# Kernel tuning notes

Measured on AMD Instinct MI355X. Metric: run time of the kernel, lower is better.

Reference implementation:

```python
import jax, jax.numpy as jnp
import numpy as np

N_NODES = 50000
N_EDGES = 200000
N_GRAPH = 1024
H = 128          # hidden_channels
POS = 48         # pos_offset
NF = 256         # num_filters in SchNetInteraction
L = 5            # n_layers
NFF = 512
MAX_ITEM = 300


def ssp(v):
    # shifted softplus used by SchNet
    return jax.nn.softplus(v) - jnp.log(2.0)


def setup_inputs() -> dict:
    key = jax.random.key(0)
    ks = iter(jax.random.split(key, 40))
    s = 0.05
    inp = {}
    inp['x'] = jax.random.randint(next(ks), (N_NODES,), 0, MAX_ITEM)
    inp['edge_index'] = jax.random.randint(next(ks), (2, N_EDGES), 0, N_NODES)
    inp['edge_attr'] = jax.random.normal(next(ks), (N_EDGES, 4), jnp.float32)
    inp['batch'] = jnp.sort(jax.random.randint(next(ks), (N_NODES,), 0, N_GRAPH))
    inp['pos'] = jax.random.normal(next(ks), (N_NODES, 3), jnp.float32)
    # embedding / projection params
    vert = jax.random.normal(next(ks), (MAX_ITEM + 1, H - POS), jnp.float32) * s
    inp['vert_emb'] = vert.at[MAX_ITEM].set(0.0)  # padding_idx
    inp['pos_w'] = jax.random.normal(next(ks), (POS, 3), jnp.float32) * s
    inp['edge_w'] = jax.random.normal(next(ks), (H, 4), jnp.float32) * s
    # per-layer SchNetInteraction params (stacked over L)
    inp['filt_w1'] = jax.random.normal(next(ks), (L, NF, H), jnp.float32) * s
    inp['filt_b1'] = jnp.zeros((L, NF), jnp.float32)
    inp['filt_w2'] = jax.random.normal(next(ks), (L, NF, NF), jnp.float32) * s
    inp['filt_b2'] = jnp.zeros((L, NF), jnp.float32)
    inp['lin1_w'] = jax.random.normal(next(ks), (L, NF, H), jnp.float32) * s
    inp['lin2_w'] = jax.random.normal(next(ks), (L, H, NF), jnp.float32) * s
    inp['lin2_b'] = jnp.zeros((L, H), jnp.float32)
    inp['lin3_w'] = jax.random.normal(next(ks), (L, H, H), jnp.float32) * s
    inp['lin3_b'] = jnp.zeros((L, H), jnp.float32)
    # per-layer edge MLP: Linear(edge_ch + in_ch -> in_ch) + Tanh
    inp['em_w'] = jax.random.normal(next(ks), (L, H, 2 * H), jnp.float32) * s
    inp['em_b'] = jnp.zeros((L, H), jnp.float32)
    # head
    inp['head_w1'] = jax.random.normal(next(ks), (NFF, H), jnp.float32) * s
    inp['head_b1'] = jnp.zeros((NFF,), jnp.float32)
    inp['head_w2'] = jax.random.normal(next(ks), (1, NFF), jnp.float32) * s
    inp['head_b2'] = jnp.zeros((1,), jnp.float32)
    return inp


def _forward(x, edge_index, edge_attr, batch, pos, vert_emb, pos_w, edge_w,
             filt_w1, filt_b1, filt_w2, filt_b2, lin1_w, lin2_w, lin2_b,
             lin3_w, lin3_b, em_w, em_b, head_w1, head_b1, head_w2, head_b2):
    n = x.shape[0]
    src, dst = edge_index[0], edge_index[1]
    h = jnp.concatenate([vert_emb[x], pos @ pos_w.T], axis=-1)  # [N, H]
    ea = edge_attr @ edge_w.T                                    # [E, H]
    for i in range(L):
        # SchNetInteraction / CFConv: per-edge filter MLP, gather, scatter-sum
        W = ssp(ea @ filt_w1[i].T + filt_b1[i]) @ filt_w2[i].T + filt_b2[i]  # [E, NF]
        hj = (h @ lin1_w[i].T)[src]                                          # [E, NF]
        agg = jax.ops.segment_sum(hj * W, dst, num_segments=n)               # [N, NF]
        out = ssp(agg @ lin2_w[i].T + lin2_b[i]) @ lin3_w[i].T + lin3_b[i]   # [N, H]
        h = jax.nn.relu(out) + h  # relu + residual skip
        # edge MLP update (always active in ResGraphModule)
        ea = jnp.tanh(jnp.concatenate([ea, h[src] + h[dst]], axis=-1) @ em_w[i].T + em_b[i]) + ea
    # global mean pool over graphs
    ssum = jax.ops.segment_sum(h, batch, num_segments=N_GRAPH)               # [G, H]
    cnt = jax.ops.segment_sum(jnp.ones((n,), h.dtype), batch, num_segments=N_GRAPH)
    g = ssum / jnp.maximum(cnt, 1.0)[:, None]
    # head: Linear -> GELU (exact, as torch default) -> Dropout(eval) -> Linear
    y = jax.nn.gelu(g @ head_w1.T + head_b1, approximate=False) @ head_w2.T + head_b2
    return y  # [G, 1]


def reference(x, edge_index, edge_attr, batch, pos, vert_emb, pos_w, edge_w,
              filt_w1, filt_b1, filt_w2, filt_b2, lin1_w, lin2_w, lin2_b,
              lin3_w, lin3_b, em_w, em_b, head_w1, head_b1, head_w2, head_b2):
    return _forward(x, edge_index, edge_attr, batch, pos, vert_emb, pos_w, edge_w,
                    filt_w1, filt_b1, filt_w2, filt_b2, lin1_w, lin2_w, lin2_b,
                    lin3_w, lin3_b, em_w, em_b, head_w1, head_b1, head_w2, head_b2)
```

## Files before the change

### kernel.cpp

```cpp
#include <hip/hip_runtime.h>
#include <hip/hip_bf16.h>
#include <math.h>

#define N_NODES 50000
#define N_EDGES 200000
#define N_GRAPH 1024
#define HC      128
#define NFC     256
#define NLAYER  5
#define NFFC    512

typedef short bf16x8 __attribute__((ext_vector_type(8)));
typedef float f4v    __attribute__((ext_vector_type(4)));

__device__ __forceinline__ float ssp_f(float x) {
  float e = __expf(-fabsf(x));
  return fmaxf(x, 0.0f) + __logf(1.0f + e) - 0.69314718055994530942f;
}
__device__ __forceinline__ float tanh_f(float x) {
  float e = __expf(2.0f * fabsf(x));
  float t = 1.0f - 2.0f * __builtin_amdgcn_rcpf(e + 1.0f);
  return copysignf(t, x);
}
__device__ __forceinline__ unsigned short f2bf(float x) {
  __bf16 b = (__bf16)x;
  return __builtin_bit_cast(unsigned short, b);
}
__device__ __forceinline__ float bf2f(unsigned short u) {
  return (float)__builtin_bit_cast(__bf16, u);
}

__device__ __forceinline__ int swzA(int row, int col) {
  return (row << 7) + (((col >> 3) ^ (row & 7)) << 3) + (col & 7);
}
__device__ __forceinline__ int swzT(int row, int col) {
  return (row << 8) + (((col >> 3) ^ (row & 7)) << 3) + (col & 7);
}

__global__ void zero_kernel(float4* __restrict__ p, int n4) {
  int i = blockIdx.x * blockDim.x + threadIdx.x;
  if (i < n4) p[i] = make_float4(0.f, 0.f, 0.f, 0.f);
}
__global__ void zeroi_kernel(int* __restrict__ p, int n) {
  int i = blockIdx.x * blockDim.x + threadIdx.x;
  if (i < n) p[i] = 0;
}

__global__ void hist_kernel(const int* __restrict__ ei, int* __restrict__ deg) {
  int e = blockIdx.x * blockDim.x + threadIdx.x;
  if (e < N_EDGES) atomicAdd(&deg[ei[N_EDGES + e]], 1);
}
__global__ void scan1_kernel(const int* __restrict__ deg, int* __restrict__ excl,
                             int* __restrict__ bsum, int n) {
  __shared__ int buf[256];
  const int tid = threadIdx.x;
  const int i = blockIdx.x * 256 + tid;
  int v = (i < n) ? deg[i] : 0;
  buf[tid] = v;
  __syncthreads();
  for (int s = 1; s < 256; s <<= 1) {
    int t = (tid >= s) ? buf[tid - s] : 0;
    __syncthreads();
    buf[tid] += t;
    __syncthreads();
  }
  if (i < n) excl[i] = buf[tid] - v;
  if (tid == 255) bsum[blockIdx.x] = buf[255];
}
__global__ void scan2_kernel(int* __restrict__ bsum, int nb) {
  __shared__ int buf[256];
  const int tid = threadIdx.x;
  int v = (tid < nb) ? bsum[tid] : 0;
  buf[tid] = v;
  __syncthreads();
  for (int s = 1; s < 256; s <<= 1) {
    int t = (tid >= s) ? buf[tid - s] : 0;
    __syncthreads();
    buf[tid] += t;
    __syncthreads();
  }
  if (tid < nb) bsum[tid] = buf[tid] - v;
}
__global__ void scan3_kernel(int* __restrict__ excl, const int* __restrict__ bsum, int n) {
  int i = blockIdx.x * 256 + threadIdx.x;
  if (i < n) excl[i] += bsum[blockIdx.x];
}
__global__ void perm_kernel(const int* __restrict__ ei, int* __restrict__ cursor,
                            int* __restrict__ perm) {
  int e = blockIdx.x * blockDim.x + threadIdx.x;
  if (e < N_EDGES) {
    int d = ei[N_EDGES + e];
    int p = atomicAdd(&cursor[d], 1);
    perm[p] = e;
  }
}
__global__ void eperm_kernel(const int* __restrict__ ei, const int* __restrict__ perm,
                             int* __restrict__ eiPs, int* __restrict__ eiPd,
                             int* __restrict__ ipos) {
  int p = blockIdx.x * blockDim.x + threadIdx.x;
  if (p < N_EDGES) {
    int e = perm[p];
    eiPs[p] = ei[e];
    eiPd[p] = ei[N_EDGES + e];
    ipos[e] = p;
  }
}

__global__ void wconv_kernel(const float* __restrict__ w,
                             unsigned short* __restrict__ hi, int n) {
  int i = blockIdx.x * blockDim.x + threadIdx.x;
  if (i < n) hi[i] = f2bf(w[i]);
}

__global__ void embed_kernel(const int* __restrict__ x, const float* __restrict__ pos,
                             const float* __restrict__ vert, const float* __restrict__ posw,
                             unsigned short* __restrict__ h) {
  int n = blockIdx.x;
  int c = threadIdx.x;
  float v;
  if (c < 80) {
    v = vert[(size_t)x[n] * 80 + c];
  } else {
    int j = c - 80;
    v = pos[n*3+0]*posw[j*3+0] + pos[n*3+1]*posw[j*3+1] + pos[n*3+2]*posw[j*3+2];
  }
  h[(size_t)n*HC + c] = f2bf(v);
}

__global__ void edgeproj_kernel(const float* __restrict__ eattr, const float* __restrict__ ew,
                                unsigned short* __restrict__ eaP,
                                const int* __restrict__ ipos) {
  int idx = blockIdx.x * blockDim.x + threadIdx.x;
  if (idx >= N_EDGES * HC) return;
  int e = idx >> 7, c = idx & 127;
  const float* a = eattr + (size_t)e*4;
  const float* w = ew + (size_t)c*4;
  eaP[(size_t)ipos[e]*HC + c] = f2bf(a[0]*w[0] + a[1]*w[1] + a[2]*w[2] + a[3]*w[3]);
}

__global__ __launch_bounds__(256, 4) void nodeup_kernel(
    float* __restrict__ agg,
    const unsigned short* __restrict__ L2h,
    const float* __restrict__ b2,
    const unsigned short* __restrict__ L3h,
    const float* __restrict__ b3,
    unsigned short* h)
{
  __shared__ unsigned short ldsS[64 * 256];

  const int tid  = threadIdx.x;
  const int m0   = blockIdx.x * 64;
  const int lane = tid & 63, wave = tid >> 6;
  const int quad = lane >> 4, l16 = lane & 15;
  const int wn = wave * 32;
  const int r  = tid >> 2;
  const int cb2 = (tid & 3) * 64;

  const bool mok = (m0 + r) < N_NODES;

  if (mok) {
    const float* ap = agg + (size_t)(m0 + r) * NFC + cb2;
#pragma unroll
    for (int g = 0; g < 8; g++) {
      float4 v0 = *(const float4*)(ap + g*8);
      float4 v1 = *(const float4*)(ap + g*8 + 4);
      unsigned short th[8];
      th[0] = f2bf(v0.x); th[1] = f2bf(v0.y); th[2] = f2bf(v0.z); th[3] = f2bf(v0.w);
      th[4] = f2bf(v1.x); th[5] = f2bf(v1.y); th[6] = f2bf(v1.z); th[7] = f2bf(v1.w);
      *(bf16x8*)&ldsS[swzT(r, cb2 + g*8)] = *(bf16x8*)th;
    }
    float4* zp = (float4*)(agg + (size_t)(m0 + r) * NFC + cb2);
    const float4 z4 = make_float4(0.f, 0.f, 0.f, 0.f);
#pragma unroll
    for (int g = 0; g < 16; g++) zp[g] = z4;
  } else {
    const bf16x8 zb = {0, 0, 0, 0, 0, 0, 0, 0};
#pragma unroll
    for (int g = 0; g < 8; g++) *(bf16x8*)&ldsS[swzT(r, cb2 + g*8)] = zb;
  }

  const f4v zf = {0.f, 0.f, 0.f, 0.f};
  f4v acc[4][2];
#pragma unroll
  for (int i = 0; i < 4; i++) { acc[i][0] = zf; acc[i][1] = zf; }

  bf16x8 bn[2];
#pragma unroll
  for (int nt = 0; nt < 2; nt++)
    bn[nt] = *(const bf16x8*)&L2h[(size_t)(wn + nt*16 + l16) * NFC + quad*8];

  __syncthreads();

  for (int kki = 0; kki < 8; kki++) {
    bf16x8 bc[2] = {bn[0], bn[1]};
    if (kki < 7) {
#pragma unroll
      for (int nt = 0; nt < 2; nt++)
        bn[nt] = *(const bf16x8*)&L2h[(size_t)(wn + nt*16 + l16) * NFC
                                      + (kki+1)*32 + quad*8];
    }
    bf16x8 a[4];
#pragma unroll
    for (int t = 0; t < 4; t++)
      a[t] = *(const bf16x8*)&ldsS[swzT(t*16 + l16, kki*32 + quad*8)];
#pragma unroll
    for (int mt = 0; mt < 4; mt++)
#pragma unroll
      for (int nt = 0; nt < 2; nt++)
        acc[mt][nt] = __builtin_amdgcn_mfma_f32_16x16x32_bf16(a[mt], bc[nt], acc[mt][nt], 0, 0, 0);
  }
  __syncthreads();

#pragma unroll
  for (int nt = 0; nt < 2; nt++) {
    const int col = wn + nt*16 + l16;
    const float bz = b2[col];
#pragma unroll
    for (int mt = 0; mt < 4; mt++) {
      const int rowb = mt*16 + quad*4;
#pragma unroll
      for (int rr = 0; rr < 4; rr++)
        ldsS[swzA(rowb+rr, col)] = f2bf(ssp_f(acc[mt][nt][rr] + bz));
    }
  }

  bf16x8 b3n[2];
#pragma unroll
  for (int nt = 0; nt < 2; nt++)
    b3n[nt] = *(const bf16x8*)&L3h[(size_t)(wn + nt*16 + l16) * HC + quad*8];

  __syncthreads();

  f4v acc2[4][2];
#pragma unroll
  for (int i = 0; i < 4; i++) { acc2[i][0] = zf; acc2[i][1] = zf; }

  for (int kki = 0; kki < 4; kki++) {
    bf16x8 bc[2] = {b3n[0], b3n[1]};
    if (kki < 3) {
#pragma unroll
      for (int nt = 0; nt < 2; nt++)
        b3n[nt] = *(const bf16x8*)&L3h[(size_t)(wn + nt*16 + l16) * HC
                                       + (kki+1)*32 + quad*8];
    }
    bf16x8 a[4];
#pragma unroll
    for (int t = 0; t < 4; t++)
      a[t] = *(const bf16x8*)&ldsS[swzA(t*16 + l16, kki*32 + quad*8)];
#pragma unroll
    for (int mt = 0; mt < 4; mt++)
#pragma unroll
      for (int nt = 0; nt < 2; nt++)
        acc2[mt][nt] = __builtin_amdgcn_mfma_f32_16x16x32_bf16(a[mt], bc[nt], acc2[mt][nt], 0, 0, 0);
  }

#pragma unroll
  for (int nt = 0; nt < 2; nt++) {
    const int ncol = wn + nt*16 + l16;
    const float bz = b3[ncol];
#pragma unroll
    for (int mt = 0; mt < 4; mt++) {
      const int mb = mt*16 + quad*4;
#pragma unroll
      for (int rr = 0; rr < 4; rr++) {
        const int m = m0 + mb + rr;
        if (m < N_NODES) {
          const size_t idx = (size_t)m * HC + ncol;
          h[idx] = f2bf(fmaxf(acc2[mt][nt][rr] + bz, 0.f) + bf2f(h[idx]));
        }
      }
    }
  }
}

__device__ __forceinline__ int sigma_row(int r) {
  return ((r >> 2) & 3) * 16 + (r >> 4) * 4 + (r & 3);
}
__global__ __launch_bounds__(256, 3) void emffs_kernel(
    unsigned short* eaP,
    const unsigned short* __restrict__ emWh, const float* __restrict__ emB,
    const unsigned short* __restrict__ l1h,
    const unsigned short* __restrict__ fw1h, const float* __restrict__ fb1,
    const unsigned short* __restrict__ fw2h, const float* __restrict__ fb2,
    const int* __restrict__ eiPs, const int* __restrict__ eiPd,
    const unsigned short* __restrict__ hfeat, float* __restrict__ agg,
    const int do_em, const int do_wb)
{
  __shared__ unsigned short ldsA[64 * 128];
  __shared__ unsigned short ldsT[64 * 256];
  __shared__ int sD[64];
  unsigned short* ldsH = ldsT;

  const int tid  = threadIdx.x;
  const int m0   = blockIdx.x * 64;
  const int lane = tid & 63, wave = tid >> 6;
  const int quad = lane >> 4, l16 = lane & 15;
  const int r = tid >> 2, cb = (tid & 3) * 32;
  const int sp = m0 + sigma_row(r);

  const int s = eiPs[sp];
  bf16x8 hreg[4];
  {
    const unsigned short* hp = hfeat + (size_t)s * HC + cb;
#pragma unroll
    for (int q = 0; q < 4; q++) hreg[q] = *(const bf16x8*)(hp + q*8);
  }
  if (tid < 64) sD[tid] = eiPd[m0 + sigma_row(tid)];

  {
    const unsigned short* ap = eaP + (size_t)sp * HC + cb;
#pragma unroll
    for (int q = 0; q < 4; q++)
      *(bf16x8*)&ldsA[swzA(r, cb + q*8)] = *(const bf16x8*)(ap + q*8);
  }

  if (do_em) {
    const int d = eiPd[sp];
    const unsigned short* dp = hfeat + (size_t)d * HC + cb;
    unsigned short th[32];
#pragma unroll
    for (int q = 0; q < 4; q++) {
      bf16x8 x2 = *(const bf16x8*)(dp + q*8);
#pragma unroll
      for (int j = 0; j < 8; j++) {
        unsigned short a16 = ((const unsigned short*)&hreg[q])[j];
        unsigned short b16 = ((const unsigned short*)&x2)[j];
        th[q*8 + j] = f2bf(bf2f(a16) + bf2f(b16));
      }
    }
#pragma unroll
    for (int q = 0; q < 4; q++)
      *(bf16x8*)&ldsH[swzA(r, cb + q*8)] = *(bf16x8*)&th[q*8];
  }

  const f4v zf = {0.f, 0.f, 0.f, 0.f};

  bf16x8 bn;
  if (do_em)
    bn = *(const bf16x8*)&emWh[(size_t)(wave*32 + l16) * 2*HC + quad*8];

  __syncthreads();

  if (do_em) {
    f4v eacc[4][2];
#pragma unroll
    for (int mt = 0; mt < 4; mt++) { eacc[mt][0] = zf; eacc[mt][1] = zf; }
#pragma unroll
    for (int g = 0; g < 16; g++) {
      const int nt = g >> 3, hf = (g >> 2) & 1, ki = g & 3;
      bf16x8 bc = bn;
      if (g < 15) {
        const int g1 = g + 1;
        const int nt1 = g1 >> 3, hf1 = (g1 >> 2) & 1, ki1 = g1 & 3;
        bn = *(const bf16x8*)&emWh[(size_t)(wave*32 + nt1*16 + l16) * 2*HC
                                   + hf1*HC + ki1*32 + quad*8];
      }
      const unsigned short* src = hf ? ldsH : ldsA;
#pragma unroll
      for (int mt = 0; mt < 4; mt++) {
        bf16x8 a = *(const bf16x8*)&src[swzA(mt*16 + l16, ki*32 + quad*8)];
        eacc[mt][nt] = __builtin_amdgcn_mfma_f32_16x16x32_bf16(a, bc, eacc[mt][nt], 0, 0, 0);
      }
    }
#pragma unroll
    for (int nt = 0; nt < 2; nt++) {
      const int col = wave*32 + nt*16 + l16;
      const float bz = emB[col];
#pragma unroll
      for (int mt = 0; mt < 4; mt++) {
        const int rowb = mt*16 + quad*4;
#pragma unroll
        for (int rr = 0; rr < 4; rr++) {
          const int row = rowb + rr;
          ldsA[swzA(row, col)] = f2bf(tanh_f(eacc[mt][nt][rr] + bz)
                                      + bf2f(ldsA[swzA(row, col)]));
        }
      }
    }
    __syncthreads();
    if (do_wb) {
      unsigned short* op = eaP + (size_t)sp * HC + cb;
#pragma unroll
      for (int q = 0; q < 4; q++)
        *(bf16x8*)(op + q*8) = *(const bf16x8*)&ldsA[swzA(r, cb + q*8)];
    }
  }

  for (int p = 0; p < 4; p++) {
    f4v tacc[4];
#pragma unroll
    for (int mt = 0; mt < 4; mt++) tacc[mt] = zf;
    const size_t b1row = (size_t)(p*64 + wave*16 + l16);
#pragma unroll
    for (int kk = 0; kk < 128; kk += 32) {
      bf16x8 b = *(const bf16x8*)&fw1h[b1row * HC + kk + quad*8];
#pragma unroll
      for (int mt = 0; mt < 4; mt++) {
        bf16x8 a = *(const bf16x8*)&ldsA[swzA(mt*16 + l16, kk + quad*8)];
        tacc[mt] = __builtin_amdgcn_mfma_f32_16x16x32_bf16(a, b, tacc[mt], 0, 0, 0);
      }
    }
    const int col = p*64 + wave*16 + l16;
    const float bz = fb1[col];
#pragma unroll
    for (int mt = 0; mt < 4; mt++) {
      const int rowb = mt*16 + quad*4;
#pragma unroll
      for (int rr = 0; rr < 4; rr++)
        ldsT[swzT(rowb+rr, col)] = f2bf(ssp_f(tacc[mt][rr] + bz));
    }
  }
  __syncthreads();

#pragma unroll
  for (int q = 0; q < 4; q++)
    *(bf16x8*)&ldsA[swzA(r, cb + q*8)] = hreg[q];
  __syncthreads();

  for (int hf = 0; hf < 2; hf++) {
    f4v wacc[4][2];
#pragma unroll
    for (int mt = 0; mt < 4; mt++) { wacc[mt][0] = zf; wacc[mt][1] = zf; }

    __builtin_amdgcn_s_setprio(1);
    for (int p = 0; p < 4; p++) {
#pragma unroll
      for (int kc = 0; kc < 2; kc++) {
        bf16x8 a_[4];
#pragma unroll
        for (int mt = 0; mt < 4; mt++)
          a_[mt] = *(const bf16x8*)&ldsT[swzT(mt*16 + l16, p*64 + kc*32 + quad*8)];
#pragma unroll
        for (int nt = 0; nt < 2; nt++) {
          const size_t brow = (size_t)(wave*64 + (hf*2 + nt)*16 + l16);
          bf16x8 b = *(const bf16x8*)&fw2h[brow * NFC + p*64 + kc*32 + quad*8];
#pragma unroll
          for (int mt = 0; mt < 4; mt++)
            wacc[mt][nt] = __builtin_amdgcn_mfma_f32_16x16x32_bf16(a_[mt], b, wacc[mt][nt], 0, 0, 0);
        }
      }
    }

    f4v hacc[4][2];
#pragma unroll
    for (int mt = 0; mt < 4; mt++) { hacc[mt][0] = zf; hacc[mt][1] = zf; }

#pragma unroll
    for (int kk = 0; kk < 128; kk += 32) {
      bf16x8 a_[4];
#pragma unroll
      for (int mt = 0; mt < 4; mt++)
        a_[mt] = *(const bf16x8*)&ldsA[swzA(mt*16 + l16, kk + quad*8)];
#pragma unroll
      for (int nt = 0; nt < 2; nt++) {
        const size_t brow = (size_t)(wave*64 + (hf*2 + nt)*16 + l16);
        bf16x8 b = *(const bf16x8*)&l1h[brow * HC + kk + quad*8];
#pragma unroll
        for (int mt = 0; mt < 4; mt++)
          hacc[mt][nt] = __builtin_amdgcn_mfma_f32_16x16x32_bf16(a_[mt], b, hacc[mt][nt], 0, 0, 0);
      }
    }
    __builtin_amdgcn_s_setprio(0);

#pragma unroll
    for (int nt = 0; nt < 2; nt++) {
      const int col = wave*64 + (hf*2 + nt)*16 + l16;
      const float bz = fb2[col];
      float accum = 0.f;
      int prev = -1;
      bool firstrun = true;
#pragma unroll
      for (int mt = 0; mt < 4; mt++) {
#pragma unroll
        for (int rr = 0; rr < 4; rr++) {
          const int prow = mt*16 + quad*4 + rr;
          const int d = sD[prow];
          const float v = (wacc[mt][nt][rr] + bz) * hacc[mt][nt][rr];
          if (d != prev) {
            if (prev >= 0) {
              if (firstrun) atomicAdd(&agg[(size_t)prev * NFC + col], accum);
              else          agg[(size_t)prev * NFC + col] = accum;
              firstrun = false;
            }
            accum = v; prev = d;
          } else {
            accum += v;
          }
        }
      }
      atomicAdd(&agg[(size_t)prev * NFC + col], accum);
    }
  }
}

__global__ __launch_bounds__(256) void poolhead_kernel(
    const int* __restrict__ batch, const unsigned short* __restrict__ h,
    const float* __restrict__ w1, const float* __restrict__ b1,
    const float* __restrict__ w2, const float* __restrict__ b2,
    float* __restrict__ y)
{
  __shared__ float gs[HC];
  __shared__ float red[256];
  const int g = blockIdx.x;
  const int tid = threadIdx.x;

  int lo = 0, hi = N_NODES;
  while (lo < hi) { int m = (lo + hi) >> 1; if (batch[m] < g) lo = m + 1; else hi = m; }
  int lo2 = lo, hi2 = N_NODES;
  while (lo2 < hi2) { int m = (lo2 + hi2) >> 1; if (batch[m] < g + 1) lo2 = m + 1; else hi2 = m; }
  const int cnt = lo2 - lo;

  if (tid < HC) {
    float s = 0.f;
    for (int i = lo; i < lo2; i++) s += bf2f(h[(size_t)i * HC + tid]);
    gs[tid] = s / (float)max(cnt, 1);
  }
  __syncthreads();

  float partial = 0.f;
  for (int f = tid; f < NFFC; f += 256) {
    float acc = b1[f];
    const float* wr = w1 + (size_t)f * HC;
#pragma unroll 8
    for (int k = 0; k < HC; k++) acc = fmaf(gs[k], wr[k], acc);
    float t = 0.5f * acc * (1.0f + erff(acc * 0.70710678118654752440f));
    partial = fmaf(t, w2[f], partial);
  }
  red[tid] = partial;
  __syncthreads();
  for (int s = 128; s > 0; s >>= 1) {
    if (tid < s) red[tid] += red[tid + s];
    __syncthreads();
  }
  if (tid == 0) y[g] = red[0] + b2[0];
}

extern "C" void kernel_launch(void* const* d_in, const int* in_sizes, int n_in,
                              void* d_out, int out_size, void* d_ws, size_t ws_size,
                              hipStream_t stream) {
  const int*   x     = (const int*)  d_in[0];
  const int*   ei    = (const int*)  d_in[1];
  const float* eattr = (const float*)d_in[2];
  const int*   batch = (const int*)  d_in[3];
  const float* pos   = (const float*)d_in[4];
  const float* vert  = (const float*)d_in[5];
  const float* posw  = (const float*)d_in[6];
  const float* edgew = (const float*)d_in[7];
  const float* fw1   = (const float*)d_in[8];
  const float* fb1   = (const float*)d_in[9];
  const float* fw2   = (const float*)d_in[10];
  const float* fb2   = (const float*)d_in[11];
  const float* l1w   = (const float*)d_in[12];
  const float* l2w   = (const float*)d_in[13];
  const float* l2b   = (const float*)d_in[14];
  const float* l3w   = (const float*)d_in[15];
  const float* l3b   = (const float*)d_in[16];
  const float* emw   = (const float*)d_in[17];
  const float* emb   = (const float*)d_in[18];
  const float* hw1   = (const float*)d_in[19];
  const float* hb1   = (const float*)d_in[20];
  const float* hw2   = (const float*)d_in[21];
  const float* hb2   = (const float*)d_in[22];
  float* out = (float*)d_out;

  char* ws = (char*)d_ws;
  size_t off = 0;
  auto alloc = [&](size_t bytes) { char* p = ws + off; off += (bytes + 511) & ~(size_t)511; return p; };
  unsigned short* eaP = (unsigned short*)alloc((size_t)N_EDGES*HC*2);
  unsigned short* h   = (unsigned short*)alloc((size_t)N_NODES*HC*2);
  float* agg  = (float*)alloc((size_t)N_NODES*NFC*4);
  int* deg    = (int*)alloc((size_t)(N_NODES+1)*4);
  int* cursor = (int*)alloc((size_t)(N_NODES+1)*4);
  int* bsum   = (int*)alloc((size_t)256*4);
  int* perm   = (int*)alloc((size_t)N_EDGES*4);
  int* eiPs   = (int*)alloc((size_t)N_EDGES*4);
  int* eiPd   = (int*)alloc((size_t)N_EDGES*4);
  int* ipos   = (int*)alloc((size_t)N_EDGES*4);
  const int n_fw1 = NLAYER*NFC*HC, n_fw2 = NLAYER*NFC*NFC, n_l1 = NLAYER*NFC*HC;
  const int n_l2 = NLAYER*HC*NFC, n_l3 = NLAYER*HC*HC, n_em = NLAYER*HC*2*HC;
  unsigned short* fw1h = (unsigned short*)alloc((size_t)n_fw1*2);
  unsigned short* fw2h = (unsigned short*)alloc((size_t)n_fw2*2);
  unsigned short* l1h  = (unsigned short*)alloc((size_t)n_l1*2);
  unsigned short* l2h  = (unsigned short*)alloc((size_t)n_l2*2);
  unsigned short* l3h  = (unsigned short*)alloc((size_t)n_l3*2);
  unsigned short* emh  = (unsigned short*)alloc((size_t)n_em*2);

  const int NSCAN = N_NODES + 1;
  const int NB    = (NSCAN + 255) / 256;

  zeroi_kernel<<<(NSCAN+255)/256, 256, 0, stream>>>(deg, NSCAN);
  hist_kernel<<<(N_EDGES+255)/256, 256, 0, stream>>>(ei, deg);
  scan1_kernel<<<NB, 256, 0, stream>>>(deg, cursor, bsum, NSCAN);
  scan2_kernel<<<1, 256, 0, stream>>>(bsum, NB);
  scan3_kernel<<<NB, 256, 0, stream>>>(cursor, bsum, NSCAN);
  perm_kernel<<<(N_EDGES+255)/256, 256, 0, stream>>>(ei, cursor, perm);
  eperm_kernel<<<(N_EDGES+255)/256, 256, 0, stream>>>(ei, perm, eiPs, eiPd, ipos);

  wconv_kernel<<<(n_fw1+255)/256, 256, 0, stream>>>(fw1, fw1h, n_fw1);
  wconv_kernel<<<(n_fw2+255)/256, 256, 0, stream>>>(fw2, fw2h, n_fw2);
  wconv_kernel<<<(n_l1 +255)/256, 256, 0, stream>>>(l1w, l1h, n_l1);
  wconv_kernel<<<(n_l2 +255)/256, 256, 0, stream>>>(l2w, l2h, n_l2);
  wconv_kernel<<<(n_l3 +255)/256, 256, 0, stream>>>(l3w, l3h, n_l3);
  wconv_kernel<<<(n_em +255)/256, 256, 0, stream>>>(emw, emh, n_em);

  const int GN   = (N_NODES + 63) / 64;
  const int GE64 = N_EDGES / 64;

  embed_kernel<<<N_NODES, 128, 0, stream>>>(x, pos, vert, posw, h);
  edgeproj_kernel<<<(N_EDGES*HC + 255)/256, 256, 0, stream>>>(eattr, edgew, eaP, ipos);
  zero_kernel<<<((N_NODES*NFC/4) + 255)/256, 256, 0, stream>>>(
      (float4*)agg, N_NODES*NFC/4);

  for (int i = 0; i < NLAYER; ++i) {
    const int em_i = (i > 0) ? (i - 1) : 0;
    emffs_kernel<<<GE64, 256, 0, stream>>>(
        eaP,
        emh + (size_t)em_i*HC*2*HC, emb + (size_t)em_i*HC,
        l1h + (size_t)i*NFC*HC,
        fw1h + (size_t)i*NFC*HC, fb1 + (size_t)i*NFC,
        fw2h + (size_t)i*NFC*NFC, fb2 + (size_t)i*NFC,
        eiPs, eiPd, h, agg, (i > 0) ? 1 : 0, (i < NLAYER - 1) ? 1 : 0);
    nodeup_kernel<<<GN, 256, 0, stream>>>(
        agg, l2h + (size_t)i*HC*NFC, l2b + (size_t)i*HC,
        l3h + (size_t)i*HC*HC, l3b + (size_t)i*HC, h);
  }

  poolhead_kernel<<<N_GRAPH, 256, 0, stream>>>(batch, h, hw1, hb1, hw2, hb2, out);
}
```

Measured before the change: 1.355 ms.

## Fuse edge projection into first layer and load edge features via LDS DMA

Removes the standalone edge-projection kernel and the inverse-permutation array. Layer 0 now computes the 4-to-128 edge projection inside the edge kernel, using perm to find each edge's original attributes, and writes the permuted result both to LDS and to global memory. Later layers load the edge features straight into LDS with global_load_lds, using a source-side XOR swizzle, instead of going through registers. This avoids one full-size edge pass and register staging, but the DMA path only works if its LDS layout matches swzA and its loads finish before the barrier.

```diff
diff --git a/kernel.cpp b/kernel.cpp
--- a/kernel.cpp
+++ b/kernel.cpp
@@ -12,6 +12,8 @@
 
 typedef short bf16x8 __attribute__((ext_vector_type(8)));
 typedef float f4v    __attribute__((ext_vector_type(4)));
+typedef __attribute__((address_space(1))) const unsigned int gu32;
+typedef __attribute__((address_space(3))) unsigned int su32;
 
 __device__ __forceinline__ float ssp_f(float x) {
   float e = __expf(-fabsf(x));
@@ -95,14 +97,12 @@
   }
 }
 __global__ void eperm_kernel(const int* __restrict__ ei, const int* __restrict__ perm,
-                             int* __restrict__ eiPs, int* __restrict__ eiPd,
-                             int* __restrict__ ipos) {
+                             int* __restrict__ eiPs, int* __restrict__ eiPd) {
   int p = blockIdx.x * blockDim.x + threadIdx.x;
   if (p < N_EDGES) {
     int e = perm[p];
     eiPs[p] = ei[e];
     eiPd[p] = ei[N_EDGES + e];
-    ipos[e] = p;
   }
 }
 
@@ -127,17 +127,6 @@
   h[(size_t)n*HC + c] = f2bf(v);
 }
 
-__global__ void edgeproj_kernel(const float* __restrict__ eattr, const float* __restrict__ ew,
-                                unsigned short* __restrict__ eaP,
-                                const int* __restrict__ ipos) {
-  int idx = blockIdx.x * blockDim.x + threadIdx.x;
-  if (idx >= N_EDGES * HC) return;
-  int e = idx >> 7, c = idx & 127;
-  const float* a = eattr + (size_t)e*4;
-  const float* w = ew + (size_t)c*4;
-  eaP[(size_t)ipos[e]*HC + c] = f2bf(a[0]*w[0] + a[1]*w[1] + a[2]*w[2] + a[3]*w[3]);
-}
-
 __global__ __launch_bounds__(256, 4) void nodeup_kernel(
     float* __restrict__ agg,
     const unsigned short* __restrict__ L2h,
@@ -284,6 +273,8 @@
     const unsigned short* __restrict__ fw2h, const float* __restrict__ fb2,
     const int* __restrict__ eiPs, const int* __restrict__ eiPd,
     const unsigned short* __restrict__ hfeat, float* __restrict__ agg,
+    const float* __restrict__ eattr, const float* __restrict__ edgew,
+    const int* __restrict__ perm,
     const int do_em, const int do_wb)
 {
   __shared__ unsigned short ldsA[64 * 128];
@@ -307,14 +298,17 @@
   }
   if (tid < 64) sD[tid] = eiPd[m0 + sigma_row(tid)];
 
-  {
-    const unsigned short* ap = eaP + (size_t)sp * HC + cb;
-#pragma unroll
-    for (int q = 0; q < 4; q++)
-      *(bf16x8*)&ldsA[swzA(r, cb + q*8)] = *(const bf16x8*)(ap + q*8);
-  }
-
   if (do_em) {
+#pragma unroll
+    for (int q = 0; q < 4; q++) {
+      const int row = 4*(wave*4 + q) + (lane >> 4);
+      const int cs  = lane & 15;
+      const int spr = m0 + sigma_row(row);
+      const unsigned short* gsrc = eaP + (size_t)spr * HC + ((cs ^ (row & 7)) << 3);
+      __builtin_amdgcn_global_load_lds(
+          (gu32*)(const void*)gsrc,
+          (su32*)(void*)&ldsA[(size_t)(wave*4 + q) * 512], 16, 0, 0);
+    }
     const int d = eiPd[sp];
     const unsigned short* dp = hfeat + (size_t)d * HC + cb;
     unsigned short th[32];
@@ -331,6 +325,22 @@
 #pragma unroll
     for (int q = 0; q < 4; q++)
       *(bf16x8*)&ldsH[swzA(r, cb + q*8)] = *(bf16x8*)&th[q*8];
+  } else {
+    const int pe = perm[sp];
+    const float4 a4 = *(const float4*)(eattr + (size_t)pe * 4);
+    unsigned short th[32];
+#pragma unroll
+    for (int j = 0; j < 32; j++) {
+      const float* w4 = edgew + (size_t)(cb + j) * 4;
+      th[j] = f2bf(a4.x*w4[0] + a4.y*w4[1] + a4.z*w4[2] + a4.w*w4[3]);
+    }
+#pragma unroll
+    for (int q = 0; q < 4; q++)
+      *(bf16x8*)&ldsA[swzA(r, cb + q*8)] = *(bf16x8*)&th[q*8];
+    unsigned short* op = eaP + (size_t)sp * HC + cb;
+#pragma unroll
+    for (int q = 0; q < 4; q++)
+      *(bf16x8*)(op + q*8) = *(bf16x8*)&th[q*8];
   }
 
   const f4v zf = {0.f, 0.f, 0.f, 0.f};
@@ -575,7 +585,6 @@
   int* perm   = (int*)alloc((size_t)N_EDGES*4);
   int* eiPs   = (int*)alloc((size_t)N_EDGES*4);
   int* eiPd   = (int*)alloc((size_t)N_EDGES*4);
-  int* ipos   = (int*)alloc((size_t)N_EDGES*4);
   const int n_fw1 = NLAYER*NFC*HC, n_fw2 = NLAYER*NFC*NFC, n_l1 = NLAYER*NFC*HC;
   const int n_l2 = NLAYER*HC*NFC, n_l3 = NLAYER*HC*HC, n_em = NLAYER*HC*2*HC;
   unsigned short* fw1h = (unsigned short*)alloc((size_t)n_fw1*2);
@@ -594,7 +603,7 @@
   scan2_kernel<<<1, 256, 0, stream>>>(bsum, NB);
   scan3_kernel<<<NB, 256, 0, stream>>>(cursor, bsum, NSCAN);
   perm_kernel<<<(N_EDGES+255)/256, 256, 0, stream>>>(ei, cursor, perm);
-  eperm_kernel<<<(N_EDGES+255)/256, 256, 0, stream>>>(ei, perm, eiPs, eiPd, ipos);
+  eperm_kernel<<<(N_EDGES+255)/256, 256, 0, stream>>>(ei, perm, eiPs, eiPd);
 
   wconv_kernel<<<(n_fw1+255)/256, 256, 0, stream>>>(fw1, fw1h, n_fw1);
   wconv_kernel<<<(n_fw2+255)/256, 256, 0, stream>>>(fw2, fw2h, n_fw2);
@@ -607,7 +616,6 @@
   const int GE64 = N_EDGES / 64;
 
   embed_kernel<<<N_NODES, 128, 0, stream>>>(x, pos, vert, posw, h);
-  edgeproj_kernel<<<(N_EDGES*HC + 255)/256, 256, 0, stream>>>(eattr, edgew, eaP, ipos);
   zero_kernel<<<((N_NODES*NFC/4) + 255)/256, 256, 0, stream>>>(
       (float4*)agg, N_NODES*NFC/4);
 
@@ -619,7 +627,9 @@
         l1h + (size_t)i*NFC*HC,
         fw1h + (size_t)i*NFC*HC, fb1 + (size_t)i*NFC,
         fw2h + (size_t)i*NFC*NFC, fb2 + (size_t)i*NFC,
-        eiPs, eiPd, h, agg, (i > 0) ? 1 : 0, (i < NLAYER - 1) ? 1 : 0);
+        eiPs, eiPd, h, agg,
+        eattr, edgew, perm,
+        (i > 0) ? 1 : 0, (i < NLAYER - 1) ? 1 : 0);
     nodeup_kernel<<<GN, 256, 0, stream>>>(
         agg, l2h + (size_t)i*HC*NFC, l2b + (size_t)i*HC,
         l3h + (size_t)i*HC*HC, l3b + (size_t)i*HC, h);
```

Result: no change. 1.365 ms (+0.7%).
